# Performance work log

Measured on AMD Instinct MI355X. Metric: run time of the kernel, lower is better.

Reference implementation:

```python
import jax, jax.numpy as jnp
import numpy as np

B, CIN, CMID, COUT, H, W = 4, 64, 128, 128, 128, 128
K = 9  # 3x3 taps
EPS = 1e-5


def conv3x3(x, w, b):
    # standard 3x3 conv, stride 1, pad 1, NCHW / OIHW
    y = jax.lax.conv_general_dilated(x, w, (1, 1), ((1, 1), (1, 1)),
                                     dimension_numbers=('NCHW', 'OIHW', 'NCHW'))
    return y + b[None, :, None, None]


def deform_conv3x3(x, offset, w, b):
    # torchvision DeformConv2d semantics (v1, no mask), kernel 3, pad 1, stride 1.
    # offset: [B, 2*K, H, W] with per-tap (dy, dx) pairs.
    Bn, C, Hn, Wn = x.shape
    off = offset.reshape(Bn, K, 2, Hn, Wn)
    off_y, off_x = off[:, :, 0], off[:, :, 1]          # [B,K,H,W]
    ky = (jnp.arange(K) // 3).astype(x.dtype)          # tap row 0..2
    kx = (jnp.arange(K) % 3).astype(x.dtype)           # tap col 0..2
    # sampling positions: p = out_pos - pad + tap + offset
    py = jnp.arange(Hn, dtype=x.dtype)[None, None, :, None] - 1.0 + ky[None, :, None, None] + off_y
    px = jnp.arange(Wn, dtype=x.dtype)[None, None, None, :] - 1.0 + kx[None, :, None, None] + off_x
    y0 = jnp.floor(py); x0 = jnp.floor(px)
    wy1 = py - y0; wx1 = px - x0                       # bilinear fractions
    y0i = y0.astype(jnp.int32); x0i = x0.astype(jnp.int32)
    xf = x.reshape(Bn, C, Hn * Wn)

    def gather(iy, ix):
        valid = ((iy >= 0) & (iy < Hn) & (ix >= 0) & (ix < Wn)).astype(x.dtype)
        idx = jnp.clip(iy, 0, Hn - 1) * Wn + jnp.clip(ix, 0, Wn - 1)  # [B,K,H,W]
        g = jax.vmap(lambda xb, ib: xb[:, ib])(xf, idx)               # [B,C,K,H,W]
        return g, valid

    g00, v00 = gather(y0i, x0i)
    g01, v01 = gather(y0i, x0i + 1)
    g10, v10 = gather(y0i + 1, x0i)
    g11, v11 = gather(y0i + 1, x0i + 1)

    def wmul(g, v, wgt):
        return g * (v * wgt)[:, None]                  # broadcast over channel dim

    sampled = (wmul(g00, v00, (1 - wy1) * (1 - wx1)) +
               wmul(g01, v01, (1 - wy1) * wx1) +
               wmul(g10, v10, wy1 * (1 - wx1)) +
               wmul(g11, v11, wy1 * wx1))              # [B,C,K,H,W]
    out = jnp.einsum('bckhw,ock->bohw', sampled, w.reshape(w.shape[0], C, K))
    return out + b[None, :, None, None]


def batchnorm_relu(x, gamma, beta):
    # training-mode BN: batch statistics over (N,H,W), biased variance
    mean = jnp.mean(x, axis=(0, 2, 3), keepdims=True)
    var = jnp.mean(jnp.square(x - mean), axis=(0, 2, 3), keepdims=True)
    y = (x - mean) * jax.lax.rsqrt(var + EPS)
    return jax.nn.relu(y * gamma[None, :, None, None] + beta[None, :, None, None])


def setup_inputs() -> dict:
    key = jax.random.key(0)
    ks = jax.random.split(key, 13)
    s = 0.05  # small weights keep offsets small / sampling mostly in-bounds
    return {
        'x': jax.random.normal(ks[0], (B, CIN, H, W), jnp.float32),
        'w_off1': jax.random.normal(ks[1], (2 * K, CIN, 3, 3), jnp.float32) * s,
        'b_off1': jnp.zeros((2 * K,), jnp.float32),
        'w1': jax.random.normal(ks[2], (CMID, CIN, 3, 3), jnp.float32) * s,
        'b1': jax.random.normal(ks[3], (CMID,), jnp.float32) * s,
        'g1': jnp.ones((CMID,), jnp.float32),
        'be1': jnp.zeros((CMID,), jnp.float32),
        'w_off2': jax.random.normal(ks[4], (2 * K, CMID, 3, 3), jnp.float32) * s,
        'b_off2': jnp.zeros((2 * K,), jnp.float32),
        'w2': jax.random.normal(ks[5], (COUT, CMID, 3, 3), jnp.float32) * s,
        'b2': jax.random.normal(ks[6], (COUT,), jnp.float32) * s,
        'g2': jnp.ones((COUT,), jnp.float32),
        'be2': jnp.zeros((COUT,), jnp.float32),
    }


def reference(x, w_off1, b_off1, w1, b1, g1, be1, w_off2, b_off2, w2, b2, g2, be2):
    offset1 = conv3x3(x, w_off1, b_off1)
    out = deform_conv3x3(x, offset1, w1, b1)
    out = batchnorm_relu(out, g1, be1)
    offset2 = conv3x3(out, w_off2, b_off2)
    out = deform_conv3x3(out, offset2, w2, b2)
    out = batchnorm_relu(out, g2, be2)
    return out
```

## Files before the change

### kernel.cpp

```cpp
#include <hip/hip_runtime.h>
#include <hip/hip_bf16.h>

#define BB 4
#define H_ 128
#define W_ 128
#define HWP 16384
#define CIN1 64
#define CMID 128
#define KOFF 18

typedef short short8 __attribute__((ext_vector_type(8)));
typedef float floatx4 __attribute__((ext_vector_type(4)));

#define WS_AB   16
#define WS_CVT  288
#define CVT_TOTAL 4447396
#define WS_WF1  4447744
#define WS_WF2  4484608
#define WS_XT   4558336
#define WS_OFF  6655488
#define WS_Y1   7835136
#define WS_Y1T  16223744
#define WS_OFFB 20418048
#define OFF_HSTRIDE (WS_OFFB - WS_OFF)
#define WS_PART 21600000
#define WS_Y2   WS_Y1

#define R_X     0
#define R_WOFF1 4194304
#define R_BOFF1 4204672
#define R_W1    4204690
#define R_B1    4278418
#define R_G1    4278546
#define R_BE1   4278674
#define R_WOFF2 4278802
#define R_BOFF2 4299538
#define R_W2    4299556
#define R_B2    4447012
#define R_G2    4447140
#define R_BE2   4447268

struct SrcPtrs { const void* p[13]; };

__device__ inline short f2bf(float f) {
    __hip_bfloat16 h = __float2bfloat16(f);
    return *reinterpret_cast<short*>(&h);
}
__device__ inline float bf2f(unsigned short u) {
    return __uint_as_float(((unsigned int)u) << 16);
}
__device__ inline float bfu_lo(unsigned int u) { return __uint_as_float(u << 16); }
__device__ inline float bfu_hi(unsigned int u) { return __uint_as_float(u & 0xFFFF0000u); }

__global__ void probe_dtype_k(const unsigned int* __restrict__ g1, int* __restrict__ flag) {
    if (threadIdx.x == 0 && blockIdx.x == 0) {
        flag[0] = ((g1[0] & 0xFFFFu) != 0u) ? 1 : 0;
    }
}

__global__ __launch_bounds__(256) void convert_inputs_k(SrcPtrs sp, float* __restrict__ dst,
                                                        const int* __restrict__ flag, int total) {
    int i = blockIdx.x * 256 + threadIdx.x;
    if (i >= total) return;
    constexpr int prefix[13] = {0, R_WOFF1, R_BOFF1, R_W1, R_B1, R_G1, R_BE1,
                                R_WOFF2, R_BOFF2, R_W2, R_B2, R_G2, R_BE2};
    const void* src = sp.p[0];
    int base = 0;
#pragma unroll
    for (int q = 1; q < 13; ++q) {
        if (i >= prefix[q]) { src = sp.p[q]; base = prefix[q]; }
    }
    int local = i - base;
    float v;
    if (flag[0] != 0) {
        v = bf2f(((const unsigned short*)src)[local]);
    } else {
        v = ((const float*)src)[local];
    }
    dst[i] = v;
}

template <int CIN>
__global__ __launch_bounds__(256) void wf_build_k(const float* __restrict__ w, short* __restrict__ wf) {
    constexpr int KSTEPS = CIN * 9 / 32;
    int idx = blockIdx.x * 256 + threadIdx.x;
    int j    = idx & 7;
    int lane = (idx >> 3) & 63;
    int rem  = idx >> 9;
    int ks   = rem % KSTEPS;
    int ct   = rem / KSTEPS;
    int co = ct * 16 + (lane & 15);
    int k  = ks * 32 + (lane >> 4) * 8 + j;
    int ci = k & (CIN - 1);
    int kk = k / CIN;
    wf[idx] = f2bf(w[(co * CIN + ci) * 9 + kk]);
}

__global__ __launch_bounds__(256) void xt_build_k(const float* __restrict__ x, unsigned short* __restrict__ xt) {
    __shared__ __align__(4) short s_t[64 * 66];
    int bi  = blockIdx.x;
    int hw0 = (bi & 255) * 64;
    int b   = bi >> 8;
    int t   = threadIdx.x;
    int hwp = t & 63;
#pragma unroll
    for (int it = 0; it < 16; ++it) {
        int c = it * 4 + (t >> 6);
        float v = x[((long)(b * 64 + c) << 14) + hw0 + hwp];
        s_t[hwp * 66 + c] = f2bf(v);
    }
    __syncthreads();
#pragma unroll
    for (int it = 0; it < 8; ++it) {
        int i  = it * 256 + t;
        int c2 = (i & 31) * 2;
        int hw2 = i >> 5;
        int sv = *(const int*)&s_t[hw2 * 66 + c2];
        *(int*)&xt[((long)((b << 14) + hw0 + hw2)) * 64 + c2] = sv;
    }
}

template <int CIN>
__global__ __launch_bounds__(256) void conv3x3_split_k(const float* __restrict__ x,
                                                       const float* __restrict__ w,
                                                       const float* __restrict__ bias,
                                                       float* __restrict__ outp) {
    constexpr int CIH = CIN / 2;
    int bi   = blockIdx.x;
    int half = bi >> 9;
    int h    = bi & 127;
    int b    = (bi >> 7) & 3;
    int t    = threadIdx.x;
    int wq   = t & 127;
    int cg   = __builtin_amdgcn_readfirstlane(t >> 7);
    int co0  = cg * 9;
    int ci0  = half * CIH;

    float acc[9];
#pragma unroll
    for (int j = 0; j < 9; ++j) acc[j] = (half == 0) ? bias[co0 + j] : 0.f;

    const float* xb = x + ((long)(b * CIN + ci0) << 14);
    bool bm = h > 0, bp = h < H_ - 1, bl = wq > 0, br = wq < W_ - 1;
    int rm = (bm ? h - 1 : 0) << 7;
    int rc = h << 7;
    int rp = (bp ? h + 1 : H_ - 1) << 7;

#pragma unroll 2
    for (int ci = 0; ci < CIH; ++ci) {
        const float* plane = xb + ((long)ci << 14);
        float v0 = plane[rm + wq - 1], v1 = plane[rm + wq], v2 = plane[rm + wq + 1];
        float v3 = plane[rc + wq - 1], v4 = plane[rc + wq], v5 = plane[rc + wq + 1];
        float v6 = plane[rp + wq - 1], v7 = plane[rp + wq], v8 = plane[rp + wq + 1];
        v0 = (bm && bl) ? v0 : 0.f;
        v1 = bm ? v1 : 0.f;
        v2 = (bm && br) ? v2 : 0.f;
        v3 = bl ? v3 : 0.f;
        v5 = br ? v5 : 0.f;
        v6 = (bp && bl) ? v6 : 0.f;
        v7 = bp ? v7 : 0.f;
        v8 = (bp && br) ? v8 : 0.f;
#pragma unroll
        for (int j = 0; j < 9; ++j) {
            const float* wk = w + ((long)(co0 + j) * CIN + ci0 + ci) * 9;
            acc[j] += v0 * wk[0] + v1 * wk[1] + v2 * wk[2]
                    + v3 * wk[3] + v4 * wk[4] + v5 * wk[5]
                    + v6 * wk[6] + v7 * wk[7] + v8 * wk[8];
        }
    }

    long ob = (long)half * OFF_HSTRIDE + ((long)(b * KOFF + co0) << 14) + (h << 7) + wq;
#pragma unroll
    for (int j = 0; j < 9; ++j) outp[ob + ((long)j << 14)] = acc[j];
}

template <int CIN>
__global__ __launch_bounds__(256) void deform_mfma_k(const unsigned short* __restrict__ xt,
                                                     const float* __restrict__ off,
                                                     const short* __restrict__ wf,
                                                     const float* __restrict__ bias,
                                                     float* __restrict__ out) {
    constexpr int K = CIN * 9;
    constexpr int PAD = K + 8;
    constexpr int KSTEPS = K / 32;
    __shared__ __align__(16) short s_samp[16 * PAD];

    int bi = blockIdx.x;
    int w0 = (bi & 7) * 16;
    int h  = (bi >> 3) & 127;
    int b  = bi >> 10;
    int t  = threadIdx.x;
    int lane = t & 63;
    int wv   = t >> 6;

    float tw0 = 0.f, tw1 = 0.f, tw2 = 0.f, tw3 = 0.f;
    int   tp0 = 0, tp1 = 0, tp2 = 0, tp3 = 0;
    if (lane < 36) {
        int r = wv + 4 * lane;
        int p = r & 15;
        int k = r >> 4;
        int wpix = w0 + p;
        long obase = ((long)(b * KOFF) << 14) + (h << 7) + wpix;
        long iy = obase + ((long)(2 * k) << 14);
        long ix = obase + ((long)(2 * k + 1) << 14);
        float oy = off[iy] + off[iy + OFF_HSTRIDE];
        float ox = off[ix] + off[ix + OFF_HSTRIDE];
        float py = (float)(h - 1 + (k / 3)) + oy;
        float px = (float)(wpix - 1 + (k % 3)) + ox;
        float fy = floorf(py), fx = floorf(px);
        float wy = py - fy, wx = px - fx;
        int y0 = (int)fy, x0 = (int)fx;
        int y1 = y0 + 1, x1 = x0 + 1;
        bool vy0 = (y0 >= 0) && (y0 < H_);
        bool vy1 = (y1 >= 0) && (y1 < H_);
        bool vx0 = (x0 >= 0) && (x0 < W_);
        bool vx1 = (x1 >= 0) && (x1 < W_);
        float wy0 = 1.f - wy, wx0 = 1.f - wx;
        tw0 = (vy0 && vx0) ? wy0 * wx0 : 0.f;
        tw1 = (vy0 && vx1) ? wy0 * wx  : 0.f;
        tw2 = (vy1 && vx0) ? wy  * wx0 : 0.f;
        tw3 = (vy1 && vx1) ? wy  * wx  : 0.f;
        int iy0 = min(max(y0, 0), H_ - 1), iy1 = min(max(y1, 0), H_ - 1);
        int ix0 = min(max(x0, 0), W_ - 1), ix1 = min(max(x1, 0), W_ - 1);
        tp0 = (iy0 * W_ + ix0) * CIN;
        tp1 = (iy0 * W_ + ix1) * CIN;
        tp2 = (iy1 * W_ + ix0) * CIN;
        tp3 = (iy1 * W_ + ix1) * CIN;
    }

    const unsigned short* xb = xt + (long)b * HWP * CIN;

#pragma unroll
    for (int i = 0; i < 36; ++i) {
        int r  = wv + 4 * i;
        int p  = r & 15;
        int kk = r >> 4;
        int i00 = __builtin_amdgcn_readlane(tp0, i);
        int i01 = __builtin_amdgcn_readlane(tp1, i);
        int i10 = __builtin_amdgcn_readlane(tp2, i);
        int i11 = __builtin_amdgcn_readlane(tp3, i);
        float w00 = __int_as_float(__builtin_amdgcn_readlane(__float_as_int(tw0), i));
        float w01 = __int_as_float(__builtin_amdgcn_readlane(__float_as_int(tw1), i));
        float w10 = __int_as_float(__builtin_amdgcn_readlane(__float_as_int(tw2), i));
        float w11 = __int_as_float(__builtin_amdgcn_readlane(__float_as_int(tw3), i));
        if constexpr (CIN == 128) {
            unsigned int u00 = *(const unsigned int*)(xb + i00 + 2 * lane);
            unsigned int u01 = *(const unsigned int*)(xb + i01 + 2 * lane);
            unsigned int u10 = *(const unsigned int*)(xb + i10 + 2 * lane);
            unsigned int u11 = *(const unsigned int*)(xb + i11 + 2 * lane);
            float vlo = w00 * bfu_lo(u00) + w01 * bfu_lo(u01) + w10 * bfu_lo(u10) + w11 * bfu_lo(u11);
            float vhi = w00 * bfu_hi(u00) + w01 * bfu_hi(u01) + w10 * bfu_hi(u10) + w11 * bfu_hi(u11);
            __hip_bfloat162 h2 = __float22bfloat162_rn(make_float2(vlo, vhi));
            *(unsigned int*)&s_samp[p * PAD + kk * CIN + 2 * lane] = *reinterpret_cast<unsigned int*>(&h2);
        } else {
            float x00 = bf2f(xb[i00 + lane]);
            float x01 = bf2f(xb[i01 + lane]);
            float x10 = bf2f(xb[i10 + lane]);
            float x11 = bf2f(xb[i11 + lane]);
            float v = w00 * x00 + w01 * x01 + w10 * x10 + w11 * x11;
            s_samp[p * PAD + kk * CIN + lane] = f2bf(v);
        }
    }
    __syncthreads();

    int p_   = lane & 15;
    int quad = lane >> 4;
    int ct0 = wv * 2, ct1 = wv * 2 + 1;

    floatx4 acc0, acc1;
#pragma unroll
    for (int r = 0; r < 4; ++r) {
        acc0[r] = bias[ct0 * 16 + quad * 4 + r];
        acc1[r] = bias[ct1 * 16 + quad * 4 + r];
    }

#pragma unroll 4
    for (int ks = 0; ks < KSTEPS; ++ks) {
        short8 bfrag = *(const short8*)&s_samp[p_ * PAD + ks * 32 + quad * 8];
        short8 a0 = *(const short8*)&wf[(((long)ct0 * KSTEPS + ks) * 64 + lane) * 8];
        short8 a1 = *(const short8*)&wf[(((long)ct1 * KSTEPS + ks) * 64 + lane) * 8];
        acc0 = __builtin_amdgcn_mfma_f32_16x16x32_bf16(a0, bfrag, acc0, 0, 0, 0);
        acc1 = __builtin_amdgcn_mfma_f32_16x16x32_bf16(a1, bfrag, acc1, 0, 0, 0);
    }

    long ob = ((long)(b * 128) << 14) + (h << 7) + w0 + p_;
#pragma unroll
    for (int r = 0; r < 4; ++r) {
        out[ob + ((long)(ct0 * 16 + quad * 4 + r) << 14)] = acc0[r];
        out[ob + ((long)(ct1 * 16 + quad * 4 + r) << 14)] = acc1[r];
    }
}

__global__ __launch_bounds__(256) void bn_stats_part_k(const float* __restrict__ y, float* __restrict__ part) {
    int bi = blockIdx.x;
    int c = bi & 127;
    int b = bi >> 7;
    int t = threadIdx.x;
    const float4* p4 = (const float4*)(y + ((long)(b * 128 + c) << 14));
    float sum = 0.f, ss = 0.f;
#pragma unroll
    for (int i = 0; i < 16; ++i) {
        float4 v = p4[t + 256 * i];
        sum += v.x + v.y + v.z + v.w;
        ss  += v.x * v.x + v.y * v.y + v.z * v.z + v.w * v.w;
    }
#pragma unroll
    for (int o = 32; o > 0; o >>= 1) { sum += __shfl_down(sum, o); ss += __shfl_down(ss, o); }
    __shared__ float s1[4], s2[4];
    int wave = t >> 6;
    if ((t & 63) == 0) { s1[wave] = sum; s2[wave] = ss; }
    __syncthreads();
    if (t == 0) {
        part[bi]       = s1[0] + s1[1] + s1[2] + s1[3];
        part[512 + bi] = s2[0] + s2[1] + s2[2] + s2[3];
    }
}

__global__ void bn_final_k(const float* __restrict__ part, const float* __restrict__ g,
                           const float* __restrict__ be, float* __restrict__ ab) {
    int c = threadIdx.x;
    float sum = 0.f, ss = 0.f;
#pragma unroll
    for (int b = 0; b < 4; ++b) {
        sum += part[b * 128 + c];
        ss  += part[512 + b * 128 + c];
    }
    float mean = sum * (1.f / 65536.f);
    float var  = ss  * (1.f / 65536.f) - mean * mean;
    float inv  = rsqrtf(var + 1e-5f);
    float a = g[c] * inv;
    ab[c]       = a;
    ab[128 + c] = be[c] - mean * a;
}

__global__ __launch_bounds__(256) void bn_apply_dual_k(float* __restrict__ y, const float* __restrict__ ab,
                                                       unsigned short* __restrict__ yt) {
    __shared__ __align__(4) short s_t[64 * 134];
    int bi  = blockIdx.x;
    int hw0 = (bi & 255) * 64;
    int b   = bi >> 8;
    int t   = threadIdx.x;
    int hwp = t & 63;
#pragma unroll 4
    for (int it = 0; it < 32; ++it) {
        int c = it * 4 + (t >> 6);
        float a = ab[c], sh = ab[128 + c];
        long addr = ((long)(b * 128 + c) << 14) + hw0 + hwp;
        float v = y[addr];
        v = fmaxf(v * a + sh, 0.f);
        y[addr] = v;
        s_t[hwp * 134 + c] = f2bf(v);
    }
    __syncthreads();
#pragma unroll 4
    for (int it = 0; it < 16; ++it) {
        int i   = it * 256 + t;
        int c2  = (i & 63) * 2;
        int hw2 = i >> 6;
        int sv = *(const int*)&s_t[hw2 * 134 + c2];
        *(int*)&yt[((long)((b << 14) + hw0 + hw2)) * 128 + c2] = sv;
    }
}

__global__ __launch_bounds__(256) void bn_apply_out_k(const float* __restrict__ y, const float* __restrict__ ab,
                                                      const int* __restrict__ flag, void* __restrict__ out, int total4) {
    int i = blockIdx.x * 256 + threadIdx.x;
    if (i >= total4) return;
    int c = (i >> 12) & 127;
    float a = ab[c], sh = ab[128 + c];
    float4 v = reinterpret_cast<const float4*>(y)[i];
    v.x = fmaxf(v.x * a + sh, 0.f);
    v.y = fmaxf(v.y * a + sh, 0.f);
    v.z = fmaxf(v.z * a + sh, 0.f);
    v.w = fmaxf(v.w * a + sh, 0.f);
    if (flag[0] != 0) {
        ushort4 u;
        u.x = (unsigned short)f2bf(v.x);
        u.y = (unsigned short)f2bf(v.y);
        u.z = (unsigned short)f2bf(v.z);
        u.w = (unsigned short)f2bf(v.w);
        reinterpret_cast<ushort4*>(out)[i] = u;
    } else {
        reinterpret_cast<float4*>(out)[i] = v;
    }
}

extern "C" void kernel_launch(void* const* d_in, const int* in_sizes, int n_in,
                              void* d_out, int out_size, void* d_ws, size_t ws_size,
                              hipStream_t stream) {
    float* ws   = (float*)d_ws;
    int*   flag = (int*)d_ws;
    float* ab   = ws + WS_AB;
    float* cvt  = ws + WS_CVT;

    const float* X     = cvt + R_X;
    const float* Woff1 = cvt + R_WOFF1;
    const float* Boff1 = cvt + R_BOFF1;
    const float* W1f   = cvt + R_W1;
    const float* B1f   = cvt + R_B1;
    const float* G1    = cvt + R_G1;
    const float* Be1   = cvt + R_BE1;
    const float* Woff2 = cvt + R_WOFF2;
    const float* Boff2 = cvt + R_BOFF2;
    const float* W2f   = cvt + R_W2;
    const float* B2f   = cvt + R_B2;
    const float* G2    = cvt + R_G2;
    const float* Be2   = cvt + R_BE2;

    short* WF1 = (short*)(ws + WS_WF1);
    short* WF2 = (short*)(ws + WS_WF2);
    unsigned short* XT  = (unsigned short*)(ws + WS_XT);
    unsigned short* Y1T = (unsigned short*)(ws + WS_Y1T);
    float* OFF  = ws + WS_OFF;
    float* PART = ws + WS_PART;
    float* Y1   = ws + WS_Y1;
    float* Y2   = ws + WS_Y2;

    SrcPtrs sp;
    for (int j = 0; j < 13; ++j) sp.p[j] = d_in[j];

    probe_dtype_k<<<1, 64, 0, stream>>>((const unsigned int*)d_in[5], flag);
    convert_inputs_k<<<(CVT_TOTAL + 255) / 256, 256, 0, stream>>>(sp, cvt, flag, CVT_TOTAL);
    wf_build_k<64><<<288, 256, 0, stream>>>(W1f, WF1);
    wf_build_k<128><<<576, 256, 0, stream>>>(W2f, WF2);
    xt_build_k<<<1024, 256, 0, stream>>>(X, XT);

    conv3x3_split_k<64><<<BB * 128 * 2, 256, 0, stream>>>(X, Woff1, Boff1, OFF);
    deform_mfma_k<64><<<BB * 128 * 8, 256, 0, stream>>>(XT, OFF, WF1, B1f, Y1);
    bn_stats_part_k<<<512, 256, 0, stream>>>(Y1, PART);
    bn_final_k<<<1, 128, 0, stream>>>(PART, G1, Be1, ab);
    bn_apply_dual_k<<<1024, 256, 0, stream>>>(Y1, ab, Y1T);

    conv3x3_split_k<128><<<BB * 128 * 2, 256, 0, stream>>>(Y1, Woff2, Boff2, OFF);
    deform_mfma_k<128><<<BB * 128 * 8, 256, 0, stream>>>(Y1T, OFF, WF2, B2f, Y2);
    bn_stats_part_k<<<512, 256, 0, stream>>>(Y2, PART);
    bn_final_k<<<1, 128, 0, stream>>>(PART, G2, Be2, ab);
    bn_apply_out_k<<<(BB * 128 * HWP / 4 + 255) / 256, 256, 0, stream>>>(Y2, ab, flag, d_out, BB * 128 * HWP / 4);
}
```

Baseline: 366.8 us.

## Pack deform gather indices and split CIN=128 deform into two LDS phases

The four per-tap gather offsets are packed into one integer (base pixel plus dx/dy bits), which cuts readlane and register use. The 128-channel deform kernel now stages the sampled tile in two phases (4 taps, then 5) through a smaller shared buffer, with MFMA accumulation between them. This lowers LDS per block and so may raise occupancy. The cost is extra barriers and less overlap between gathering and MFMA. The 64-channel kernel is split out and its MFMA loop unroll changes from 4 to 3.

After: 359.0 us. 1.02x faster.

```diff
diff --git a/kernel.cpp b/kernel.cpp
--- a/kernel.cpp
+++ b/kernel.cpp
@@ -51,6 +51,9 @@
 }
 __device__ inline float bfu_lo(unsigned int u) { return __uint_as_float(u << 16); }
 __device__ inline float bfu_hi(unsigned int u) { return __uint_as_float(u & 0xFFFF0000u); }
+__device__ inline float rl_f(float v, int i) {
+    return __int_as_float(__builtin_amdgcn_readlane(__float_as_int(v), i));
+}
 
 __global__ void probe_dtype_k(const unsigned int* __restrict__ g1, int* __restrict__ flag) {
     if (threadIdx.x == 0 && blockIdx.x == 0) {
@@ -175,26 +178,10 @@
 }
 
 template <int CIN>
-__global__ __launch_bounds__(256) void deform_mfma_k(const unsigned short* __restrict__ xt,
-                                                     const float* __restrict__ off,
-                                                     const short* __restrict__ wf,
-                                                     const float* __restrict__ bias,
-                                                     float* __restrict__ out) {
-    constexpr int K = CIN * 9;
-    constexpr int PAD = K + 8;
-    constexpr int KSTEPS = K / 32;
-    __shared__ __align__(16) short s_samp[16 * PAD];
-
-    int bi = blockIdx.x;
-    int w0 = (bi & 7) * 16;
-    int h  = (bi >> 3) & 127;
-    int b  = bi >> 10;
-    int t  = threadIdx.x;
-    int lane = t & 63;
-    int wv   = t >> 6;
-
-    float tw0 = 0.f, tw1 = 0.f, tw2 = 0.f, tw3 = 0.f;
-    int   tp0 = 0, tp1 = 0, tp2 = 0, tp3 = 0;
+__device__ inline void build_table(const float* __restrict__ off, int b, int h, int w0,
+                                   int lane, int wv,
+                                   int& tpk, float& tw0, float& tw1, float& tw2, float& tw3) {
+    tpk = 0; tw0 = tw1 = tw2 = tw3 = 0.f;
     if (lane < 36) {
         int r = wv + 4 * lane;
         int p = r & 15;
@@ -222,61 +209,154 @@
         tw3 = (vy1 && vx1) ? wy  * wx  : 0.f;
         int iy0 = min(max(y0, 0), H_ - 1), iy1 = min(max(y1, 0), H_ - 1);
         int ix0 = min(max(x0, 0), W_ - 1), ix1 = min(max(x1, 0), W_ - 1);
-        tp0 = (iy0 * W_ + ix0) * CIN;
-        tp1 = (iy0 * W_ + ix1) * CIN;
-        tp2 = (iy1 * W_ + ix0) * CIN;
-        tp3 = (iy1 * W_ + ix1) * CIN;
-    }
-
+        int dx = ix1 - ix0;
+        int dy = iy1 - iy0;
+        tpk = (iy0 * W_ + ix0) | (dx << 14) | (dy << 15);
+    }
+}
+
+template <int CIN>
+__device__ inline void gather_row(const unsigned short* __restrict__ xb, short* __restrict__ s_samp,
+                                  int PADc, int colbase, int i, int p, int kk0loc,
+                                  int lane, int tpk, float tw0, float tw1, float tw2, float tw3) {
+    int pk  = __builtin_amdgcn_readlane(tpk, i);
+    float w00 = rl_f(tw0, i), w01 = rl_f(tw1, i), w10 = rl_f(tw2, i), w11 = rl_f(tw3, i);
+    const unsigned short* b00 = xb + (pk & 0x3FFF) * CIN;
+    const unsigned short* b01 = b00 + ((pk >> 14) & 1) * CIN;
+    const unsigned short* b10 = b00 + ((pk >> 15) & 1) * (W_ * CIN);
+    const unsigned short* b11 = b01 + ((pk >> 15) & 1) * (W_ * CIN);
+    if constexpr (CIN == 128) {
+        unsigned int u00 = *(const unsigned int*)(b00 + 2 * lane);
+        unsigned int u01 = *(const unsigned int*)(b01 + 2 * lane);
+        unsigned int u10 = *(const unsigned int*)(b10 + 2 * lane);
+        unsigned int u11 = *(const unsigned int*)(b11 + 2 * lane);
+        float vlo = w00 * bfu_lo(u00) + w01 * bfu_lo(u01) + w10 * bfu_lo(u10) + w11 * bfu_lo(u11);
+        float vhi = w00 * bfu_hi(u00) + w01 * bfu_hi(u01) + w10 * bfu_hi(u10) + w11 * bfu_hi(u11);
+        __hip_bfloat162 h2 = __float22bfloat162_rn(make_float2(vlo, vhi));
+        *(unsigned int*)&s_samp[p * PADc + colbase + 2 * lane] = *reinterpret_cast<unsigned int*>(&h2);
+    } else {
+        float v = w00 * bf2f(b00[lane]) + w01 * bf2f(b01[lane])
+                + w10 * bf2f(b10[lane]) + w11 * bf2f(b11[lane]);
+        s_samp[p * PADc + colbase + lane] = f2bf(v);
+    }
+}
+
+__global__ __launch_bounds__(256) void deform_mfma64_k(const unsigned short* __restrict__ xt,
+                                                       const float* __restrict__ off,
+                                                       const short* __restrict__ wf,
+                                                       const float* __restrict__ bias,
+                                                       float* __restrict__ out) {
+    constexpr int CIN = 64;
+    constexpr int K = 576;
+    constexpr int PADc = K + 8;
+    constexpr int KSTEPS = K / 32;
+    __shared__ __align__(16) short s_samp[16 * PADc];
+
+    int bi = blockIdx.x;
+    int w0 = (bi & 7) * 16;
+    int h  = (bi >> 3) & 127;
+    int b  = bi >> 10;
+    int t  = threadIdx.x;
+    int lane = t & 63;
+    int wv   = t >> 6;
+
+    int tpk; float tw0, tw1, tw2, tw3;
+    build_table<CIN>(off, b, h, w0, lane, wv, tpk, tw0, tw1, tw2, tw3);
     const unsigned short* xb = xt + (long)b * HWP * CIN;
 
 #pragma unroll
     for (int i = 0; i < 36; ++i) {
-        int r  = wv + 4 * i;
-        int p  = r & 15;
-        int kk = r >> 4;
-        int i00 = __builtin_amdgcn_readlane(tp0, i);
-        int i01 = __builtin_amdgcn_readlane(tp1, i);
-        int i10 = __builtin_amdgcn_readlane(tp2, i);
-        int i11 = __builtin_amdgcn_readlane(tp3, i);
-        float w00 = __int_as_float(__builtin_amdgcn_readlane(__float_as_int(tw0), i));
-        float w01 = __int_as_float(__builtin_amdgcn_readlane(__float_as_int(tw1), i));
-        float w10 = __int_as_float(__builtin_amdgcn_readlane(__float_as_int(tw2), i));
-        float w11 = __int_as_float(__builtin_amdgcn_readlane(__float_as_int(tw3), i));
-        if constexpr (CIN == 128) {
-            unsigned int u00 = *(const unsigned int*)(xb + i00 + 2 * lane);
-            unsigned int u01 = *(const unsigned int*)(xb + i01 + 2 * lane);
-            unsigned int u10 = *(const unsigned int*)(xb + i10 + 2 * lane);
-            unsigned int u11 = *(const unsigned int*)(xb + i11 + 2 * lane);
-            float vlo = w00 * bfu_lo(u00) + w01 * bfu_lo(u01) + w10 * bfu_lo(u10) + w11 * bfu_lo(u11);
-            float vhi = w00 * bfu_hi(u00) + w01 * bfu_hi(u01) + w10 * bfu_hi(u10) + w11 * bfu_hi(u11);
-            __hip_bfloat162 h2 = __float22bfloat162_rn(make_float2(vlo, vhi));
-            *(unsigned int*)&s_samp[p * PAD + kk * CIN + 2 * lane] = *reinterpret_cast<unsigned int*>(&h2);
-        } else {
-            float x00 = bf2f(xb[i00 + lane]);
-            float x01 = bf2f(xb[i01 + lane]);
-            float x10 = bf2f(xb[i10 + lane]);
-            float x11 = bf2f(xb[i11 + lane]);
-            float v = w00 * x00 + w01 * x01 + w10 * x10 + w11 * x11;
-            s_samp[p * PAD + kk * CIN + lane] = f2bf(v);
-        }
+        int r = wv + 4 * i;
+        gather_row<CIN>(xb, s_samp, PADc, (r >> 4) * CIN, i, r & 15, 0,
+                        lane, tpk, tw0, tw1, tw2, tw3);
     }
     __syncthreads();
 
     int p_   = lane & 15;
     int quad = lane >> 4;
     int ct0 = wv * 2, ct1 = wv * 2 + 1;
-
     floatx4 acc0, acc1;
 #pragma unroll
     for (int r = 0; r < 4; ++r) {
         acc0[r] = bias[ct0 * 16 + quad * 4 + r];
         acc1[r] = bias[ct1 * 16 + quad * 4 + r];
     }
-
+#pragma unroll 3
+    for (int ks = 0; ks < KSTEPS; ++ks) {
+        short8 bfrag = *(const short8*)&s_samp[p_ * PADc + ks * 32 + quad * 8];
+        short8 a0 = *(const short8*)&wf[(((long)ct0 * KSTEPS + ks) * 64 + lane) * 8];
+        short8 a1 = *(const short8*)&wf[(((long)ct1 * KSTEPS + ks) * 64 + lane) * 8];
+        acc0 = __builtin_amdgcn_mfma_f32_16x16x32_bf16(a0, bfrag, acc0, 0, 0, 0);
+        acc1 = __builtin_amdgcn_mfma_f32_16x16x32_bf16(a1, bfrag, acc1, 0, 0, 0);
+    }
+
+    long ob = ((long)(b * 128) << 14) + (h << 7) + w0 + p_;
+#pragma unroll
+    for (int r = 0; r < 4; ++r) {
+        out[ob + ((long)(ct0 * 16 + quad * 4 + r) << 14)] = acc0[r];
+        out[ob + ((long)(ct1 * 16 + quad * 4 + r) << 14)] = acc1[r];
+    }
+}
+
+__global__ __launch_bounds__(256) void deform_mfma128_k(const unsigned short* __restrict__ xt,
+                                                        const float* __restrict__ off,
+                                                        const short* __restrict__ wf,
+                                                        const float* __restrict__ bias,
+                                                        float* __restrict__ out) {
+    constexpr int CIN = 128;
+    constexpr int KSTEPS = 36;
+    constexpr int PADc = 5 * 128 + 8;
+    __shared__ __align__(16) short s_samp[16 * PADc];
+
+    int bi = blockIdx.x;
+    int w0 = (bi & 7) * 16;
+    int h  = (bi >> 3) & 127;
+    int b  = bi >> 10;
+    int t  = threadIdx.x;
+    int lane = t & 63;
+    int wv   = t >> 6;
+
+    int tpk; float tw0, tw1, tw2, tw3;
+    build_table<CIN>(off, b, h, w0, lane, wv, tpk, tw0, tw1, tw2, tw3);
+    const unsigned short* xb = xt + (long)b * HWP * CIN;
+
+    int p_   = lane & 15;
+    int quad = lane >> 4;
+    int ct0 = wv * 2, ct1 = wv * 2 + 1;
+    floatx4 acc0, acc1;
+#pragma unroll
+    for (int r = 0; r < 4; ++r) {
+        acc0[r] = bias[ct0 * 16 + quad * 4 + r];
+        acc1[r] = bias[ct1 * 16 + quad * 4 + r];
+    }
+
+#pragma unroll
+    for (int j = 0; j < 16; ++j) {
+        int r = wv + 4 * j;
+        gather_row<CIN>(xb, s_samp, PADc, (r >> 4) * CIN, j, r & 15, 0,
+                        lane, tpk, tw0, tw1, tw2, tw3);
+    }
+    __syncthreads();
 #pragma unroll 4
-    for (int ks = 0; ks < KSTEPS; ++ks) {
-        short8 bfrag = *(const short8*)&s_samp[p_ * PAD + ks * 32 + quad * 8];
+    for (int ks = 0; ks < 16; ++ks) {
+        short8 bfrag = *(const short8*)&s_samp[p_ * PADc + ks * 32 + quad * 8];
+        short8 a0 = *(const short8*)&wf[(((long)ct0 * KSTEPS + ks) * 64 + lane) * 8];
+        short8 a1 = *(const short8*)&wf[(((long)ct1 * KSTEPS + ks) * 64 + lane) * 8];
+        acc0 = __builtin_amdgcn_mfma_f32_16x16x32_bf16(a0, bfrag, acc0, 0, 0, 0);
+        acc1 = __builtin_amdgcn_mfma_f32_16x16x32_bf16(a1, bfrag, acc1, 0, 0, 0);
+    }
+    __syncthreads();
+
+#pragma unroll
+    for (int j = 16; j < 36; ++j) {
+        int r = wv + 4 * j;
+        gather_row<CIN>(xb, s_samp, PADc, ((r >> 4) - 4) * CIN, j, r & 15, 0,
+                        lane, tpk, tw0, tw1, tw2, tw3);
+    }
+    __syncthreads();
+#pragma unroll 4
+    for (int ks = 16; ks < 36; ++ks) {
+        short8 bfrag = *(const short8*)&s_samp[p_ * PADc + (ks - 16) * 32 + quad * 8];
         short8 a0 = *(const short8*)&wf[(((long)ct0 * KSTEPS + ks) * 64 + lane) * 8];
         short8 a1 = *(const short8*)&wf[(((long)ct1 * KSTEPS + ks) * 64 + lane) * 8];
         acc0 = __builtin_amdgcn_mfma_f32_16x16x32_bf16(a0, bfrag, acc0, 0, 0, 0);
@@ -426,13 +506,13 @@
     xt_build_k<<<1024, 256, 0, stream>>>(X, XT);
 
     conv3x3_split_k<64><<<BB * 128 * 2, 256, 0, stream>>>(X, Woff1, Boff1, OFF);
-    deform_mfma_k<64><<<BB * 128 * 8, 256, 0, stream>>>(XT, OFF, WF1, B1f, Y1);
+    deform_mfma64_k<<<BB * 128 * 8, 256, 0, stream>>>(XT, OFF, WF1, B1f, Y1);
     bn_stats_part_k<<<512, 256, 0, stream>>>(Y1, PART);
     bn_final_k<<<1, 128, 0, stream>>>(PART, G1, Be1, ab);
     bn_apply_dual_k<<<1024, 256, 0, stream>>>(Y1, ab, Y1T);
 
     conv3x3_split_k<128><<<BB * 128 * 2, 256, 0, stream>>>(Y1, Woff2, Boff2, OFF);
-    deform_mfma_k<128><<<BB * 128 * 8, 256, 0, stream>>>(Y1T, OFF, WF2, B2f, Y2);
+    deform_mfma128_k<<<BB * 128 * 8, 256, 0, stream>>>(Y1T, OFF, WF2, B2f, Y2);
     bn_stats_part_k<<<512, 256, 0, stream>>>(Y2, PART);
     bn_final_k<<<1, 128, 0, stream>>>(PART, G2, Be2, ab);
     bn_apply_out_k<<<(BB * 128 * HWP / 4 + 255) / 256, 256, 0, stream>>>(Y2, ab, flag, d_out, BB * 128 * HWP / 4);
```
